# Optimization experiments

Measured on AMD Instinct MI355X. Metric: run time of the kernel, lower is better.

Reference implementation:

```python
import jax, jax.numpy as jnp
import numpy as np


def gcn(adj_bin, x, W, b):
    # torch_geometric GCNConv with add_self_loops=True, no edge_weight (binary adj)
    N = adj_bin.shape[-1]
    A = adj_bin + jnp.eye(N, dtype=adj_bin.dtype)
    d = A.sum(-1)
    dis = jnp.where(d > 0, jax.lax.rsqrt(jnp.maximum(d, 1e-12)), 0.0)
    norm = dis[..., :, None] * A * dis[..., None, :]
    return jnp.einsum('bij,bjh->bih', norm, x @ W) + b


def normalize_batch_adj(adj):
    # CoarsenBlock.normalize_batch_adj on weighted dense adjacency
    N = adj.shape[-1]
    A = adj + jnp.eye(N, dtype=adj.dtype)
    dis = jnp.clip(A.sum(-1), 1.0, None) ** -0.5
    newA = dis[..., :, None] * A * dis[..., None, :]
    return (adj.sum(-1) > 0).astype(adj.dtype)[..., None] * newA


def cut_and_mask(alpha, num_sent, k):
    # get_topk_range_for_sentences: walk alpha in descending order until k
    # indices that are sentence nodes (index < num_sent) have been seen.
    N = alpha.shape[0]
    order = jnp.argsort(-alpha)  # descending
    csum = jnp.cumsum((order < num_sent).astype(jnp.int32))
    pos = jnp.argmax(csum >= k)  # first position where k sentences seen
    cut = alpha[order[pos]]
    sorted_mask = (jnp.arange(N) <= pos).astype(alpha.dtype)
    index_mask = jnp.zeros_like(alpha).at[order].set(sorted_mask)
    return cut, index_mask


def setup_inputs() -> dict:
    key = jax.random.key(0)
    ks = jax.random.split(key, 8)
    B, N, F, H = 16, 1024, 768, 128
    x = jax.random.normal(ks[0], (B, N, F), jnp.float32)
    w = jax.random.uniform(ks[1], (B, N, N), jnp.float32)
    m = jax.random.uniform(ks[2], (B, N, N)) < 0.03  # ~30 avg degree
    adj = jnp.where(m, w, 0.0)
    num_sentences = jax.random.randint(ks[3], (B,), 4, N + 1).astype(jnp.int32)
    W1 = jax.random.normal(ks[4], (F, H), jnp.float32) / np.float32(np.sqrt(F))
    b1 = jnp.zeros((H,), jnp.float32)
    Watt = jax.random.normal(ks[5], (H, 1), jnp.float32) / np.float32(np.sqrt(H))
    batt = jnp.zeros((1,), jnp.float32)
    W2 = jax.random.normal(ks[6], (H, F), jnp.float32) / np.float32(np.sqrt(H))
    b2 = jnp.zeros((F,), jnp.float32)
    return dict(x=x, adj=adj, num_sentences=num_sentences, W1=W1, b1=b1,
                Watt=Watt, batt=batt, W2=W2, b2=b2, num_output_sentences=3)


def reference(x, adj, num_sentences, W1, b1, Watt, batt, W2, b2, num_output_sentences):
    adj_bin = (adj > 0).astype(x.dtype)
    # embed_block1 + relu
    x1 = jax.nn.relu(gcn(adj_bin, x, W1, b1))  # [B,N,H]
    # attention: sigmoid(gcn_att(x1)^2)
    alpha = jax.nn.sigmoid(gcn(adj_bin, x1, Watt, batt) ** 2)[..., 0]  # [B,N]
    norm_adj = normalize_batch_adj(adj)  # [B,N,N]
    cut, index_mask = jax.vmap(cut_and_mask, in_axes=(0, 0, None))(
        alpha, num_sentences, num_output_sentences)
    cut_alpha = jax.nn.relu(alpha + 1e-7 - cut[:, None])  # [B,N]
    S = norm_adj * cut_alpha[:, None, :]
    # F.normalize(S, p=1, dim=-1)
    S = S / jnp.clip(jnp.abs(S).sum(-1, keepdims=True), 1e-12, None)
    # coarsening matmuls
    coarse_x = jnp.einsum('bij,bif->bjf', S, x1)        # S^T x1
    StA = jnp.einsum('bji,bjk->bik', S, adj)            # S^T A
    coarse_adj = jnp.einsum('bik,bkl->bil', StA, S)     # S^T A S
    coarse_adj = jnp.floor(coarse_adj * 1e4) / 1e4      # floor quantization, 4 digits
    # embed_block2 + tanh on the coarse graph (binary coarse adjacency)
    coarse_bin = (coarse_adj != 0).astype(x.dtype)
    x2 = jnp.tanh(gcn(coarse_bin, coarse_x, W2, b2))    # [B,N,F]
    xs0 = coarse_x.mean(-1)
    xs1 = x2.mean(-1)
    return (x2, coarse_x, coarse_adj, S, index_mask, xs0, xs1)
```

## Files before the change

### kernel.cpp

```cpp
#include <hip/hip_runtime.h>

#define B_ 16
#define N_ 1024
#define F_ 768
#define H_ 128

typedef float f32x4 __attribute__((ext_vector_type(4)));
typedef short s16x8 __attribute__((ext_vector_type(8)));
typedef unsigned short u16;
typedef u16 u16x8 __attribute__((ext_vector_type(8)));
typedef u16 u16x4 __attribute__((ext_vector_type(4)));
typedef unsigned long long u64;

__device__ __forceinline__ u16 f2b(float f) {
  unsigned u = __float_as_uint(f);
  unsigned r = (u + 0x7FFFu + ((u >> 16) & 1u)) >> 16;
  return (u16)r;
}
__device__ __forceinline__ float b2f(u16 u) {
  return __uint_as_float(((unsigned)u) << 16);
}

__device__ __forceinline__ void gload16(const u16* g, u16* l) {
  __builtin_amdgcn_global_load_lds(
      (const __attribute__((address_space(1))) unsigned int*)g,
      (__attribute__((address_space(3))) unsigned int*)l, 16, 0, 0);
}

__device__ __forceinline__ float ftanh(float z) {
  z = fminf(fmaxf(z, -10.0f), 10.0f);
  float e = __expf(2.0f * z);
  return (e - 1.0f) / (e + 1.0f);
}

__device__ __forceinline__ float blockReduceSum256(float v) {
  __shared__ float red[4];
  #pragma unroll
  for (int o = 32; o > 0; o >>= 1) v += __shfl_down(v, o, 64);
  if ((threadIdx.x & 63) == 0) red[threadIdx.x >> 6] = v;
  __syncthreads();
  float r = red[0] + red[1] + red[2] + red[3];
  __syncthreads();
  return r;
}

__global__ __launch_bounds__(256) void k_prep(
    const float* __restrict__ W1, u16* __restrict__ W1h,
    u16* __restrict__ W1m, u16* __restrict__ W1l,
    const float* __restrict__ adj, float* __restrict__ dis_bin,
    float* __restrict__ dr, float* __restrict__ dc, u64* __restrict__ bm,
    u16* __restrict__ adj_bf, int* __restrict__ rowcnt,
    float* __restrict__ xs0, float* __restrict__ xs1) {
  __shared__ float tile[32][33];
  int tid = threadIdx.x;
  if (blockIdx.x < 96) {
    int bid = blockIdx.x;
    int bx = bid & 3, by = bid >> 2;
    int tx = tid & 31, ty = tid >> 5;
    int r0 = by * 32, c0 = bx * 32;
    #pragma unroll
    for (int i = 0; i < 4; ++i)
      tile[ty + i * 8][tx] = W1[(long)(r0 + ty + i * 8) * H_ + (c0 + tx)];
    __syncthreads();
    #pragma unroll
    for (int i = 0; i < 4; ++i) {
      float v = tile[tx][ty + i * 8];
      long o = (long)(c0 + ty + i * 8) * F_ + (r0 + tx);
      u16 h = f2b(v); float r1 = v - b2f(h);
      u16 m = f2b(r1); float r2 = r1 - b2f(m);
      u16 l = f2b(r2);
      W1h[o] = h; W1m[o] = m; W1l[o] = l;
    }
  } else {
    long row = blockIdx.x - 96;
    const float* a = adj + row * N_;
    u16* ab = adj_bf + row * N_;
    float cnt = 0.f, sw = 0.f;
    #pragma unroll
    for (int it = 0; it < 4; ++it) {
      int j = tid + it * 256;
      float v = a[j];
      ab[j] = f2b(v);
      bool nz = (v != 0.0f);
      u64 ball = __ballot(nz);
      if ((tid & 63) == 0) bm[row * 16 + it * 4 + (tid >> 6)] = ball;
      if (nz) { cnt += 1.0f; sw += v; }
    }
    __shared__ float r1[4], r2[4];
    #pragma unroll
    for (int o = 32; o > 0; o >>= 1) { cnt += __shfl_down(cnt, o, 64); sw += __shfl_down(sw, o, 64); }
    if ((tid & 63) == 0) { r1[tid >> 6] = cnt; r2[tid >> 6] = sw; }
    __syncthreads();
    if (tid == 0) {
      float c = r1[0] + r1[1] + r1[2] + r1[3];
      float s = r2[0] + r2[1] + r2[2] + r2[3];
      dis_bin[row] = rsqrtf(c + 1.0f);
      float d = rsqrtf(s + 1.0f);
      dc[row] = d;
      dr[row] = (s > 0.0f) ? d : 0.0f;
      rowcnt[row] = 0;
      xs0[row] = 0.0f;
      xs1[row] = 0.0f;
    }
  }
}

__global__ __launch_bounds__(256) void mgemmG1(
    const float* __restrict__ X,
    const u16* __restrict__ B0, const u16* __restrict__ B1,
    const u16* __restrict__ B2, float* __restrict__ C) {
  int m0 = blockIdx.y * 128, n0 = blockIdx.x * 64;
  __shared__ __align__(16) u16 As[3][128 * 40];
  __shared__ __align__(16) u16 Bs[3][64 * 32];
  int tid = threadIdx.x;
  int lane = tid & 63, wave = tid >> 6;
  int wr = wave >> 1, wc = wave & 1;
  int kg = lane >> 4, r16 = lane & 15;
  int arow = tid >> 1, ahalf = (tid & 1) * 16;
  const float* gx = X + (long)(m0 + arow) * F_ + ahalf;
  const u16* gb[3] = {
      B0 + (long)(n0 + (tid >> 2)) * F_ + (tid & 3) * 8,
      B1 + (long)(n0 + (tid >> 2)) * F_ + (tid & 3) * 8,
      B2 + (long)(n0 + (tid >> 2)) * F_ + (tid & 3) * 8};
  f32x4 acc[4][2] = {};

  for (int k0 = 0; k0 < F_; k0 += 32) {
    #pragma unroll
    for (int p2 = 0; p2 < 3; ++p2)
      gload16(gb[p2] + k0, &Bs[p2][tid * 8]);
    #pragma unroll
    for (int q = 0; q < 4; ++q) {
      f32x4 v = *(const f32x4*)(gx + k0 + q * 4);
      u16x4 oh, om, ol;
      #pragma unroll
      for (int e = 0; e < 4; ++e) {
        float f = v[e];
        u16 h = f2b(f); float rr1 = f - b2f(h);
        u16 m = f2b(rr1); float rr2 = rr1 - b2f(m);
        u16 l = f2b(rr2);
        oh[e] = h; om[e] = m; ol[e] = l;
      }
      int off = arow * 40 + ahalf + q * 4;
      *(u16x4*)(&As[0][off]) = oh;
      *(u16x4*)(&As[1][off]) = om;
      *(u16x4*)(&As[2][off]) = ol;
    }
    __syncthreads();
    s16x8 af[3][4], bf[3][2];
    #pragma unroll
    for (int p2 = 0; p2 < 3; ++p2) {
      #pragma unroll
      for (int m = 0; m < 4; ++m)
        af[p2][m] = *(const s16x8*)(&As[p2][(wr * 64 + m * 16 + r16) * 40 + kg * 8]);
      #pragma unroll
      for (int n = 0; n < 2; ++n)
        bf[p2][n] = *(const s16x8*)(&Bs[p2][(wc * 32 + n * 16 + r16) * 32 + kg * 8]);
    }
    #pragma unroll
    for (int m = 0; m < 4; ++m)
      #pragma unroll
      for (int n = 0; n < 2; ++n) {
        acc[m][n] = __builtin_amdgcn_mfma_f32_16x16x32_bf16(af[0][m], bf[0][n], acc[m][n], 0, 0, 0);
        acc[m][n] = __builtin_amdgcn_mfma_f32_16x16x32_bf16(af[0][m], bf[1][n], acc[m][n], 0, 0, 0);
        acc[m][n] = __builtin_amdgcn_mfma_f32_16x16x32_bf16(af[1][m], bf[0][n], acc[m][n], 0, 0, 0);
        acc[m][n] = __builtin_amdgcn_mfma_f32_16x16x32_bf16(af[1][m], bf[1][n], acc[m][n], 0, 0, 0);
        acc[m][n] = __builtin_amdgcn_mfma_f32_16x16x32_bf16(af[0][m], bf[2][n], acc[m][n], 0, 0, 0);
        acc[m][n] = __builtin_amdgcn_mfma_f32_16x16x32_bf16(af[2][m], bf[0][n], acc[m][n], 0, 0, 0);
      }
    __syncthreads();
  }

  #pragma unroll
  for (int m = 0; m < 4; ++m)
    #pragma unroll
    for (int r = 0; r < 4; ++r) {
      int row = m0 + wr * 64 + m * 16 + kg * 4 + r;
      #pragma unroll
      for (int n = 0; n < 2; ++n) {
        int col = n0 + wc * 32 + n * 16 + r16;
        C[(long)row * H_ + col] = acc[m][n][r];
      }
    }
}

__global__ __launch_bounds__(256) void k_G5G6(
    const u16* __restrict__ St, const u16* __restrict__ x1T,
    float* __restrict__ out_cx, u16* __restrict__ cx_bf,
    float* __restrict__ xs0,
    const u16* __restrict__ adjBF, u16* __restrict__ M1t) {
  __shared__ __align__(16) u16 smem[128 * 64];
  const long NN = (long)N_ * N_;
  const long NH = (long)N_ * H_;
  int tid = threadIdx.x;
  int lane = tid & 63, wave = tid >> 6;
  int wr = wave >> 1, wc = wave & 1;
  int kg = lane >> 4, r16 = lane & 15;

  if ((int)blockIdx.x < 256) {
    int id = blockIdx.x;
    int bxg = id & 1, byg = (id >> 1) & 7, bz = id >> 4;
    int m0 = byg * 128, n0 = bxg * 64;
    u16* As = smem;
    u16* Bs = smem + 128 * 32;
    const u16* ga = St + (long)bz * NN + (long)(m0 + (tid >> 2)) * N_ + (tid & 3) * 8;
    const u16* gb = x1T + (long)bz * NH + (long)(n0 + (tid >> 2)) * N_ + (tid & 3) * 8;
    f32x4 acc[4][2] = {};
    for (int k0 = 0; k0 < N_; k0 += 32) {
      gload16(ga + k0, &As[tid * 8]);
      gload16(ga + (long)64 * N_ + k0, &As[2048 + tid * 8]);
      gload16(gb + k0, &Bs[tid * 8]);
      __syncthreads();
      s16x8 af[4], bf[2];
      #pragma unroll
      for (int m = 0; m < 4; ++m)
        af[m] = *(const s16x8*)(&As[(wr * 64 + m * 16 + r16) * 32 + kg * 8]);
      #pragma unroll
      for (int n = 0; n < 2; ++n)
        bf[n] = *(const s16x8*)(&Bs[(wc * 32 + n * 16 + r16) * 32 + kg * 8]);
      #pragma unroll
      for (int m = 0; m < 4; ++m)
        #pragma unroll
        for (int n = 0; n < 2; ++n)
          acc[m][n] = __builtin_amdgcn_mfma_f32_16x16x32_bf16(af[m], bf[n], acc[m][n], 0, 0, 0);
      __syncthreads();
    }
    #pragma unroll
    for (int m = 0; m < 4; ++m)
      #pragma unroll
      for (int r = 0; r < 4; ++r) {
        int row = m0 + wr * 64 + m * 16 + kg * 4 + r;
        float part = 0.f;
        #pragma unroll
        for (int n = 0; n < 2; ++n) {
          int col = n0 + wc * 32 + n * 16 + r16;
          long cidx = (long)bz * NH + (long)row * H_ + col;
          float v = acc[m][n][r];
          out_cx[cidx] = v;
          cx_bf[cidx] = f2b(v);
          part += v;
        }
        #pragma unroll
        for (int o2 = 1; o2 < 16; o2 <<= 1) part += __shfl_xor(part, o2, 64);
        if (r16 == 0) atomicAdd(&xs0[(long)bz * N_ + row], part * (1.0f / H_));
      }
  } else {
    int lin = (int)blockIdx.x - 256;
    int swz = (lin & 7) * 128 + (lin >> 3);
    int bx = swz & 7, by = (swz >> 3) & 7, bz = swz >> 6;
    int m0 = by * 128, n0 = bx * 128;
    u16* As = smem;
    u16* Bs = smem + 128 * 32;
    const u16* ga = St + (long)bz * NN + (long)(m0 + (tid >> 2)) * N_ + (tid & 3) * 8;
    const u16* gb = adjBF + (long)bz * NN + (long)(n0 + (tid >> 2)) * N_ + (tid & 3) * 8;
    f32x4 acc[4][4] = {};
    for (int k0 = 0; k0 < N_; k0 += 32) {
      gload16(ga + k0, &As[tid * 8]);
      gload16(ga + (long)64 * N_ + k0, &As[2048 + tid * 8]);
      gload16(gb + k0, &Bs[tid * 8]);
      gload16(gb + (long)64 * N_ + k0, &Bs[2048 + tid * 8]);
      __syncthreads();
      s16x8 af[4], bfr[4];
      #pragma unroll
      for (int m = 0; m < 4; ++m)
        af[m] = *(const s16x8*)(&As[(wr * 64 + m * 16 + r16) * 32 + kg * 8]);
      #pragma unroll
      for (int n = 0; n < 4; ++n)
        bfr[n] = *(const s16x8*)(&Bs[(wc * 64 + n * 16 + r16) * 32 + kg * 8]);
      #pragma unroll
      for (int m = 0; m < 4; ++m)
        #pragma unroll
        for (int n = 0; n < 4; ++n)
          acc[m][n] = __builtin_amdgcn_mfma_f32_16x16x32_bf16(af[m], bfr[n], acc[m][n], 0, 0, 0);
      __syncthreads();
    }
    #pragma unroll
    for (int m = 0; m < 4; ++m)
      #pragma unroll
      for (int r = 0; r < 4; ++r) {
        int row = m0 + wr * 64 + m * 16 + kg * 4 + r;
        #pragma unroll
        for (int n = 0; n < 4; ++n) {
          int col = n0 + wc * 64 + n * 16 + r16;
          M1t[(long)bz * NN + (long)row * N_ + col] = f2b(acc[m][n][r]);
        }
      }
  }
}

__global__ __launch_bounds__(256) void k_spmm_relu(
    const u64* __restrict__ bm, const float* __restrict__ P1,
    const float* __restrict__ dis_bin, const float* __restrict__ b1,
    const float* __restrict__ Watt, float* __restrict__ x1,
    float* __restrict__ t) {
  long row = blockIdx.x;
  int b = (int)(row >> 10), i = (int)(row & 1023);
  const float* Pb = P1 + (long)b * (long)N_ * H_;
  const float* db = dis_bin + (long)b * N_;
  __shared__ int idxs[N_];
  __shared__ int wtot[4];
  __shared__ float accs[8][H_];
  int tid = threadIdx.x;
  int wid = tid >> 6, lane = tid & 63;
  int base = tid * 4;
  u64 word = bm[row * 16 + (tid >> 4)];
  int sh = base & 63;
  int f0 = (int)((word >> sh) & 1), f1 = (int)((word >> (sh + 1)) & 1);
  int f2 = (int)((word >> (sh + 2)) & 1), f3 = (int)((word >> (sh + 3)) & 1);
  int c0 = f0 + f1 + f2 + f3;
  int inc = c0;
  #pragma unroll
  for (int o = 1; o < 64; o <<= 1) {
    int v = __shfl_up(inc, o, 64);
    if (lane >= o) inc += v;
  }
  if (lane == 63) wtot[wid] = inc;
  __syncthreads();
  int wbase = 0;
  #pragma unroll
  for (int w = 0; w < 4; ++w) wbase += (w < wid) ? wtot[w] : 0;
  int pos = wbase + inc - c0;
  int n = wtot[0] + wtot[1] + wtot[2] + wtot[3];
  if (f0) idxs[pos++] = base;
  if (f1) idxs[pos++] = base + 1;
  if (f2) idxs[pos++] = base + 2;
  if (f3) idxs[pos++] = base + 3;
  __syncthreads();
  int tm = tid >> 5, c4 = (tid & 31) * 4;
  f32x4 acc4 = {0.f, 0.f, 0.f, 0.f};
  for (int u = tm; u < n; u += 8) {
    int j = idxs[u];
    float w = db[j];
    f32x4 pv = *(const f32x4*)(Pb + (long)j * H_ + c4);
    acc4[0] += w * pv[0];
    acc4[1] += w * pv[1];
    acc4[2] += w * pv[2];
    acc4[3] += w * pv[3];
  }
  *(f32x4*)(&accs[tm][c4]) = acc4;
  __syncthreads();
  float v = 0.f;
  if (tid < H_) {
    int c = tid;
    float tot = 0.f;
    #pragma unroll
    for (int t8 = 0; t8 < 8; ++t8) tot += accs[t8][c];
    float di = db[i];
    tot += di * Pb[(long)i * H_ + c];
    v = fmaxf(di * tot + b1[c], 0.0f);
    x1[row * H_ + c] = v;
  }
  float prod = (tid < H_) ? v * Watt[tid] : 0.f;
  float s = blockReduceSum256(prod);
  if (tid == 0) t[row] = s;
}

__global__ __launch_bounds__(256) void k_alpha(
    const u64* __restrict__ bm, const float* __restrict__ dis_bin,
    const float* __restrict__ t, const float* __restrict__ batt,
    float* __restrict__ alpha) {
  long row = blockIdx.x;
  int b = (int)(row >> 10), i = (int)(row & 1023);
  const float* db = dis_bin + (long)b * N_;
  const float* tb = t + (long)b * N_;
  int tid = threadIdx.x;
  float s = 0.f;
  #pragma unroll
  for (int it = 0; it < 4; ++it) {
    int j = tid + it * 256;
    u64 word = bm[row * 16 + (j >> 6)];
    if ((word >> (j & 63)) & 1) s += db[j] * tb[j];
  }
  s = blockReduceSum256(s);
  if (tid == 0) {
    float di = db[i];
    float pre = di * (s + di * tb[i]) + batt[0];
    float z = pre * pre;
    alpha[row] = 1.0f / (1.0f + expf(-z));
  }
}

__global__ __launch_bounds__(1024) void k_cutmask2(
    const float* __restrict__ alpha, const int* __restrict__ num_sent,
    const int* __restrict__ nout, float* __restrict__ index_mask,
    float* __restrict__ ca) {
  int b = blockIdx.x, tid = threadIdx.x;
  __shared__ u64 keys[N_];
  __shared__ u64 red[N_];
  int ns = num_sent[b];
  float av = alpha[(long)b * N_ + tid];
  unsigned bits = __float_as_uint(av);
  u64 keyFull = ((u64)bits << 32) | (u64)(0xFFFFFFFFu - (unsigned)tid);
  keys[tid] = (tid < ns) ? keyFull : 0ULL;
  __syncthreads();
  int k = nout[0];
  u64 cutkey = 0;
  for (int r = 0; r < k; ++r) {
    red[tid] = keys[tid];
    __syncthreads();
    for (int off = 512; off > 0; off >>= 1) {
      if (tid < off) { u64 o = red[tid + off]; if (o > red[tid]) red[tid] = o; }
      __syncthreads();
    }
    u64 mx = red[0];
    __syncthreads();
    if (r == k - 1) cutkey = mx;
    else if (keys[tid] == mx) keys[tid] = 0ULL;
    __syncthreads();
  }
  float cutalpha = __uint_as_float((unsigned)(cutkey >> 32));
  index_mask[(long)b * N_ + tid] = (keyFull >= cutkey) ? 1.0f : 0.0f;
  ca[(long)b * N_ + tid] = fmaxf(av + 1e-7f - cutalpha, 0.0f);
}

__global__ __launch_bounds__(256) void k_build_S(
    const u16* __restrict__ abf, const float* __restrict__ dr,
    const float* __restrict__ dc, const float* __restrict__ ca,
    float* __restrict__ S) {
  long row = blockIdx.x;
  int b = (int)(row >> 10), i = (int)(row & 1023);
  const u16* a = abf + row * N_;
  const float* dcb = dc + (long)b * N_;
  const float* cab = ca + (long)b * N_;
  float dri = dr[row];
  int tid = threadIdx.x;
  u16x4 av4 = *(const u16x4*)(a + tid * 4);
  f32x4 dc4 = *(const f32x4*)(dcb + tid * 4);
  f32x4 ca4 = *(const f32x4*)(cab + tid * 4);
  float ls = 0.f;
  f32x4 pv;
  #pragma unroll
  for (int e = 0; e < 4; ++e) {
    int j = tid * 4 + e;
    float avv = b2f(av4[e]) + ((j == i) ? 1.0f : 0.0f);
    float v = dri * avv * dc4[e] * ca4[e];
    pv[e] = v;
    ls += v;
  }
  float sum = blockReduceSum256(ls);
  float denom = fmaxf(sum, 1e-12f);
  f32x4 out;
  #pragma unroll
  for (int e = 0; e < 4; ++e) out[e] = pv[e] / denom;
  *(f32x4*)(&S[row * N_ + tid * 4]) = out;
}

__device__ __forceinline__ void convT_body(
    const float* __restrict__ Xb, u16* __restrict__ Yb, int R, int C,
    int r0, int c0, float tile[32][33]) {
  int tx = threadIdx.x & 31, ty = threadIdx.x >> 5;
  #pragma unroll
  for (int i = 0; i < 4; ++i)
    tile[ty + i * 8][tx] = Xb[(long)(r0 + ty + i * 8) * C + (c0 + tx)];
  __syncthreads();
  #pragma unroll
  for (int i = 0; i < 4; ++i)
    Yb[(long)(c0 + ty + i * 8) * R + (r0 + tx)] = f2b(tile[tx][ty + i * 8]);
}

__global__ __launch_bounds__(256) void k_convTall(
    const float* __restrict__ S, u16* __restrict__ St,
    const float* __restrict__ x1, u16* __restrict__ x1T,
    const float* __restrict__ W2, u16* __restrict__ W2T) {
  __shared__ float tile[32][33];
  long NN = (long)N_ * N_;
  long NH = (long)N_ * H_;
  int id = blockIdx.x;
  if (id < 16384) {
    int bx = id & 31, by = (id >> 5) & 31, bz = id >> 10;
    convT_body(S + (long)bz * NN, St + (long)bz * NN, N_, N_, by * 32, bx * 32, tile);
  } else if (id < 18432) {
    int id2 = id - 16384;
    int bx = id2 & 3, by = (id2 >> 2) & 31, bz = id2 >> 7;
    convT_body(x1 + (long)bz * NH, x1T + (long)bz * NH, N_, H_, by * 32, bx * 32, tile);
  } else {
    int id3 = id - 18432;
    int bx = id3 % 24, by = id3 / 24;
    convT_body(W2, W2T, H_, F_, by * 32, bx * 32, tile);
  }
}

template<int MODE>
__global__ __launch_bounds__(256) void mgemm(
    const u16* __restrict__ A, const u16* __restrict__ Bt, void* __restrict__ Cv,
    int M, int N, int K, long sA, long sB, long sC, long ldb,
    const int* __restrict__ cnt, const float* __restrict__ bias,
    int* __restrict__ rowcnt, u16* __restrict__ cbin,
    float* __restrict__ xsum) {
  int gx = gridDim.x, gy = gridDim.y;
  int lin = (blockIdx.z * gy + blockIdx.y) * gx + blockIdx.x;
  int total = gx * gy * gridDim.z;
  int chunk = total >> 3;
  int swz = (lin & 7) * chunk + (lin >> 3);
  int bx = swz % gx; int t2 = swz / gx; int by = t2 % gy; int bz = t2 / gy;

  int m0 = by * 128, n0 = bx * 128;
  const u16* Ab = A + (long)bz * sA + (long)m0 * K;
  const u16* Bb = Bt + (long)bz * sB + (long)n0 * ldb;
  __shared__ __align__(16) u16 As[128 * 32];
  __shared__ __align__(16) u16 Bs[128 * 32];
  int tid = threadIdx.x;
  int lane = tid & 63, wave = tid >> 6;
  int wr = wave >> 1, wc = wave & 1;
  int kg = lane >> 4, r16 = lane & 15;
  const u16* ga = Ab + (long)(tid >> 2) * K + (tid & 3) * 8;
  const u16* gb = Bb + (long)(tid >> 2) * ldb + (tid & 3) * 8;
  f32x4 acc[4][4] = {};

  for (int k0 = 0; k0 < K; k0 += 32) {
    gload16(ga + k0, &As[tid * 8]);
    gload16(ga + (long)64 * K + k0, &As[2048 + tid * 8]);
    gload16(gb + k0, &Bs[tid * 8]);
    gload16(gb + (long)64 * ldb + k0, &Bs[2048 + tid * 8]);
    __syncthreads();
    s16x8 af[4], bfr[4];
    #pragma unroll
    for (int m = 0; m < 4; ++m)
      af[m] = *(const s16x8*)(&As[(wr * 64 + m * 16 + r16) * 32 + kg * 8]);
    #pragma unroll
    for (int n = 0; n < 4; ++n)
      bfr[n] = *(const s16x8*)(&Bs[(wc * 64 + n * 16 + r16) * 32 + kg * 8]);
    #pragma unroll
    for (int m = 0; m < 4; ++m)
      #pragma unroll
      for (int n = 0; n < 4; ++n)
        acc[m][n] = __builtin_amdgcn_mfma_f32_16x16x32_bf16(af[m], bfr[n], acc[m][n], 0, 0, 0);
    __syncthreads();
  }

  if constexpr (MODE == 2) {
    int* cntl = (int*)As;
    if (tid < 128) cntl[tid] = 0;
    __syncthreads();
    #pragma unroll
    for (int m = 0; m < 4; ++m) {
      #pragma unroll
      for (int r = 0; r < 4; ++r) {
        int lrow = wr * 64 + m * 16 + kg * 4 + r;
        int row = m0 + lrow;
        int nz = 0;
        #pragma unroll
        for (int n = 0; n < 4; ++n) {
          int col = n0 + wc * 64 + n * 16 + r16;
          float q = floorf(acc[m][n][r] * 10000.0f) / 10000.0f;
          long cidx = (long)bz * sC + (long)row * N + col;
          ((float*)Cv)[cidx] = q;
          bool qnz = (q != 0.0f);
          u16 bv;
          if (row == col) bv = qnz ? (u16)0x4000 : (u16)0x3F80;
          else            bv = qnz ? (u16)0x3F80 : (u16)0;
          cbin[cidx] = bv;
          nz += qnz ? 1 : 0;
        }
        atomicAdd(&cntl[lrow], nz);
      }
    }
    __syncthreads();
    if (tid < 128) atomicAdd(&rowcnt[(long)bz * N_ + m0 + tid], cntl[tid]);
    return;
  }

  #pragma unroll
  for (int m = 0; m < 4; ++m) {
    #pragma unroll
    for (int r = 0; r < 4; ++r) {
      int row = m0 + wr * 64 + m * 16 + kg * 4 + r;
      float sc = 0.f;
      if constexpr (MODE == 3)
        sc = rsqrtf(1.0f + (float)cnt[(long)bz * N_ + row]);
      float part = 0.f;
      #pragma unroll
      for (int n = 0; n < 4; ++n) {
        int col = n0 + wc * 64 + n * 16 + r16;
        float v = acc[m][n][r];
        long cidx = (long)bz * sC + (long)row * N + col;
        if constexpr (MODE == 3) {
          float th = ftanh(sc * v + bias[col]);
          ((float*)Cv)[cidx] = th;
          part += th;
        } else if constexpr (MODE == 5) {
          float scc = rsqrtf(1.0f + (float)cnt[col]);
          ((u16*)Cv)[cidx] = f2b(scc * v);
        } else {
          ((float*)Cv)[cidx] = v;
        }
      }
      if constexpr (MODE == 3) {
        #pragma unroll
        for (int o2 = 1; o2 < 16; o2 <<= 1) part += __shfl_xor(part, o2, 64);
        if (r16 == 0) atomicAdd(&xsum[(long)bz * N_ + row], part * (1.0f / F_));
      }
    }
  }
}

extern "C" void kernel_launch(void* const* d_in, const int* in_sizes, int n_in,
                              void* d_out, int out_size, void* d_ws, size_t ws_size,
                              hipStream_t stream) {
  const float* x     = (const float*)d_in[0];
  const float* adj   = (const float*)d_in[1];
  const int*   nsent = (const int*)d_in[2];
  const float* W1    = (const float*)d_in[3];
  const float* b1    = (const float*)d_in[4];
  const float* Watt  = (const float*)d_in[5];
  const float* batt  = (const float*)d_in[6];
  const float* W2    = (const float*)d_in[7];
  const float* b2    = (const float*)d_in[8];
  const int*   nout  = (const int*)d_in[9];

  const long NN = (long)N_ * N_;
  const long NH = (long)N_ * H_;
  const long NF = (long)N_ * F_;
  const int BN = B_ * N_;

  float* out_x2   = (float*)d_out;
  float* out_cx   = out_x2 + (long)B_ * NF;
  float* out_cadj = out_cx + (long)B_ * NH;
  float* out_S    = out_cadj + (long)B_ * NN;
  float* out_im   = out_S + (long)B_ * NN;
  float* out_xs0  = out_im + BN;
  float* out_xs1  = out_xs0 + BN;

  char* wsb = (char*)d_ws;
  float* P1      = (float*)wsb;
  float* x1      = P1 + (long)B_ * NH;
  float* t       = x1 + (long)B_ * NH;
  float* alpha   = t + BN;
  float* dis_bin = alpha + BN;
  float* dr      = dis_bin + BN;
  float* dc      = dr + BN;
  float* ca      = dc + BN;
  int*   rowcnt  = (int*)(ca + BN);
  u64*   bm      = (u64*)(rowcnt + BN);
  char*  p       = (char*)(bm + (long)BN * 16);
  p = (char*)(((size_t)p + 255) & ~(size_t)255);
  u16* W1h   = (u16*)p;  p += (long)H_ * F_ * 2;
  u16* W1m   = (u16*)p;  p += (long)H_ * F_ * 2;
  u16* W1l   = (u16*)p;  p += (long)H_ * F_ * 2;
  u16* W2T   = (u16*)p;  p += (long)H_ * F_ * 2;
  u16* PT    = (u16*)p;  p += (long)B_ * NH * 2;
  u16* St    = (u16*)p;  p += (long)B_ * NN * 2;
  u16* wsB   = (u16*)p;  p += (long)B_ * NN * 2;
  u16* cx_bf = (u16*)P1;
  u16* x1T   = PT;
  u16* adjBF = (u16*)out_cadj;
  u16* cbin  = wsB;
  u16* P2T   = St;
  u16* M1t   = (u16*)out_x2;

  k_prep<<<dim3(96 + BN), dim3(256), 0, stream>>>(
      W1, W1h, W1m, W1l,
      adj, dis_bin, dr, dc, bm, adjBF, rowcnt, out_xs0, out_xs1);

  mgemmG1<<<dim3(H_ / 64, BN / 128, 1), dim3(256), 0, stream>>>(
      x, W1h, W1m, W1l, P1);

  k_spmm_relu<<<dim3(BN), dim3(256), 0, stream>>>(bm, P1, dis_bin, b1, Watt, x1, t);

  k_alpha<<<dim3(BN), dim3(256), 0, stream>>>(bm, dis_bin, t, batt, alpha);
  k_cutmask2<<<dim3(B_), dim3(1024), 0, stream>>>(alpha, nsent, nout, out_im, ca);
  k_build_S<<<dim3(BN), dim3(256), 0, stream>>>(adjBF, dr, dc, ca, out_S);

  k_convTall<<<dim3(16384 + 2048 + 96), dim3(256), 0, stream>>>(
      out_S, St, x1, x1T, W2, W2T);

  k_G5G6<<<dim3(256 + 1024), dim3(256), 0, stream>>>(
      St, x1T, out_cx, cx_bf, out_xs0, adjBF, M1t);

  mgemm<2><<<dim3(N_ / 128, N_ / 128, B_), dim3(256), 0, stream>>>(
      St, M1t, out_cadj, N_, N_, N_, NN, NN, NN, N_, nullptr, nullptr, rowcnt,
      cbin, nullptr);

  mgemm<5><<<dim3(BN / 128, F_ / 128, 1), dim3(256), 0, stream>>>(
      W2T, cx_bf, P2T, F_, BN, H_, 0, 0, 0, H_, rowcnt, nullptr, nullptr,
      nullptr, nullptr);

  mgemm<3><<<dim3(F_ / 128, N_ / 128, B_), dim3(256), 0, stream>>>(
      cbin, P2T, out_x2, N_, F_, N_, NN, N_, NF, (long)BN, rowcnt, b2,
      nullptr, nullptr, out_xs1);
}
```

Before: 355.5 us.

## Fuse alpha computation into cut/mask kernel and halve G1 GEMM M-tile

```diff
diff --git a/kernel.cpp b/kernel.cpp
--- a/kernel.cpp
+++ b/kernel.cpp
@@ -109,27 +109,27 @@
     const float* __restrict__ X,
     const u16* __restrict__ B0, const u16* __restrict__ B1,
     const u16* __restrict__ B2, float* __restrict__ C) {
-  int m0 = blockIdx.y * 128, n0 = blockIdx.x * 64;
-  __shared__ __align__(16) u16 As[3][128 * 40];
+  int m0 = blockIdx.y * 64, n0 = blockIdx.x * 64;
+  __shared__ __align__(16) u16 As[3][64 * 40];
   __shared__ __align__(16) u16 Bs[3][64 * 32];
   int tid = threadIdx.x;
   int lane = tid & 63, wave = tid >> 6;
   int wr = wave >> 1, wc = wave & 1;
   int kg = lane >> 4, r16 = lane & 15;
-  int arow = tid >> 1, ahalf = (tid & 1) * 16;
-  const float* gx = X + (long)(m0 + arow) * F_ + ahalf;
+  int arow = tid >> 2, aq = (tid & 3) * 8;
+  const float* gx = X + (long)(m0 + arow) * F_ + aq;
   const u16* gb[3] = {
       B0 + (long)(n0 + (tid >> 2)) * F_ + (tid & 3) * 8,
       B1 + (long)(n0 + (tid >> 2)) * F_ + (tid & 3) * 8,
       B2 + (long)(n0 + (tid >> 2)) * F_ + (tid & 3) * 8};
-  f32x4 acc[4][2] = {};
+  f32x4 acc[2][2] = {};
 
   for (int k0 = 0; k0 < F_; k0 += 32) {
     #pragma unroll
     for (int p2 = 0; p2 < 3; ++p2)
       gload16(gb[p2] + k0, &Bs[p2][tid * 8]);
     #pragma unroll
-    for (int q = 0; q < 4; ++q) {
+    for (int q = 0; q < 2; ++q) {
       f32x4 v = *(const f32x4*)(gx + k0 + q * 4);
       u16x4 oh, om, ol;
       #pragma unroll
@@ -140,24 +140,24 @@
         u16 l = f2b(rr2);
         oh[e] = h; om[e] = m; ol[e] = l;
       }
-      int off = arow * 40 + ahalf + q * 4;
+      int off = arow * 40 + aq + q * 4;
       *(u16x4*)(&As[0][off]) = oh;
       *(u16x4*)(&As[1][off]) = om;
       *(u16x4*)(&As[2][off]) = ol;
     }
     __syncthreads();
-    s16x8 af[3][4], bf[3][2];
+    s16x8 af[3][2], bf[3][2];
     #pragma unroll
     for (int p2 = 0; p2 < 3; ++p2) {
       #pragma unroll
-      for (int m = 0; m < 4; ++m)
-        af[p2][m] = *(const s16x8*)(&As[p2][(wr * 64 + m * 16 + r16) * 40 + kg * 8]);
+      for (int m = 0; m < 2; ++m)
+        af[p2][m] = *(const s16x8*)(&As[p2][(wr * 32 + m * 16 + r16) * 40 + kg * 8]);
       #pragma unroll
       for (int n = 0; n < 2; ++n)
         bf[p2][n] = *(const s16x8*)(&Bs[p2][(wc * 32 + n * 16 + r16) * 32 + kg * 8]);
     }
     #pragma unroll
-    for (int m = 0; m < 4; ++m)
+    for (int m = 0; m < 2; ++m)
       #pragma unroll
       for (int n = 0; n < 2; ++n) {
         acc[m][n] = __builtin_amdgcn_mfma_f32_16x16x32_bf16(af[0][m], bf[0][n], acc[m][n], 0, 0, 0);
@@ -171,10 +171,10 @@
   }
 
   #pragma unroll
-  for (int m = 0; m < 4; ++m)
+  for (int m = 0; m < 2; ++m)
     #pragma unroll
     for (int r = 0; r < 4; ++r) {
-      int row = m0 + wr * 64 + m * 16 + kg * 4 + r;
+      int row = m0 + wr * 32 + m * 16 + kg * 4 + r;
       #pragma unroll
       for (int n = 0; n < 2; ++n) {
         int col = n0 + wc * 32 + n * 16 + r16;
@@ -354,40 +354,36 @@
   if (tid == 0) t[row] = s;
 }
 
-__global__ __launch_bounds__(256) void k_alpha(
+__global__ __launch_bounds__(1024) void k_alphacut(
     const u64* __restrict__ bm, const float* __restrict__ dis_bin,
     const float* __restrict__ t, const float* __restrict__ batt,
-    float* __restrict__ alpha) {
-  long row = blockIdx.x;
-  int b = (int)(row >> 10), i = (int)(row & 1023);
-  const float* db = dis_bin + (long)b * N_;
-  const float* tb = t + (long)b * N_;
-  int tid = threadIdx.x;
-  float s = 0.f;
-  #pragma unroll
-  for (int it = 0; it < 4; ++it) {
-    int j = tid + it * 256;
-    u64 word = bm[row * 16 + (j >> 6)];
-    if ((word >> (j & 63)) & 1) s += db[j] * tb[j];
-  }
-  s = blockReduceSum256(s);
-  if (tid == 0) {
-    float di = db[i];
-    float pre = di * (s + di * tb[i]) + batt[0];
-    float z = pre * pre;
-    alpha[row] = 1.0f / (1.0f + expf(-z));
-  }
-}
-
-__global__ __launch_bounds__(1024) void k_cutmask2(
-    const float* __restrict__ alpha, const int* __restrict__ num_sent,
-    const int* __restrict__ nout, float* __restrict__ index_mask,
-    float* __restrict__ ca) {
+    const int* __restrict__ num_sent, const int* __restrict__ nout,
+    float* __restrict__ index_mask, float* __restrict__ ca) {
   int b = blockIdx.x, tid = threadIdx.x;
   __shared__ u64 keys[N_];
   __shared__ u64 red[N_];
+  __shared__ float dt[N_];
+  float di = dis_bin[(long)b * N_ + tid];
+  float ti = t[(long)b * N_ + tid];
+  dt[tid] = di * ti;
+  __syncthreads();
+  float s = 0.f;
+  const u64* bmr = bm + ((long)b * N_ + tid) * 16;
+  #pragma unroll
+  for (int w = 0; w < 16; ++w) {
+    u64 word = bmr[w];
+    int base = w * 64;
+    while (word) {
+      int j = (int)__builtin_ctzll(word);
+      word &= word - 1;
+      s += dt[base + j];
+    }
+  }
+  float pre = di * (s + di * ti) + batt[0];
+  float z = pre * pre;
+  float av = 1.0f / (1.0f + expf(-z));
+
   int ns = num_sent[b];
-  float av = alpha[(long)b * N_ + tid];
   unsigned bits = __float_as_uint(av);
   u64 keyFull = ((u64)bits << 32) | (u64)(0xFFFFFFFFu - (unsigned)tid);
   keys[tid] = (tid < ns) ? keyFull : 0ULL;
@@ -646,18 +642,20 @@
   u16* cbin  = wsB;
   u16* P2T   = St;
   u16* M1t   = (u16*)out_x2;
+  (void)alpha;
 
   k_prep<<<dim3(96 + BN), dim3(256), 0, stream>>>(
       W1, W1h, W1m, W1l,
       adj, dis_bin, dr, dc, bm, adjBF, rowcnt, out_xs0, out_xs1);
 
-  mgemmG1<<<dim3(H_ / 64, BN / 128, 1), dim3(256), 0, stream>>>(
+  mgemmG1<<<dim3(H_ / 64, BN / 64, 1), dim3(256), 0, stream>>>(
       x, W1h, W1m, W1l, P1);
 
   k_spmm_relu<<<dim3(BN), dim3(256), 0, stream>>>(bm, P1, dis_bin, b1, Watt, x1, t);
 
-  k_alpha<<<dim3(BN), dim3(256), 0, stream>>>(bm, dis_bin, t, batt, alpha);
-  k_cutmask2<<<dim3(B_), dim3(1024), 0, stream>>>(alpha, nsent, nout, out_im, ca);
+  k_alphacut<<<dim3(B_), dim3(1024), 0, stream>>>(
+      bm, dis_bin, t, batt, nsent, nout, out_im, ca);
+
   k_build_S<<<dim3(BN), dim3(256), 0, stream>>>(adjBF, dr, dc, ca, out_S);
 
   k_convTall<<<dim3(16384 + 2048 + 96), dim3(256), 0, stream>>>(
```

Result: faster. 331.0 us (-6.9%).
